# Kernel optimization log

Measured on AMD Instinct MI355X. Metric: run time of the kernel, lower is better.

## Reference

```python
import jax, jax.numpy as jnp
import numpy as np

PAD = 1  # symmetric spatial padding (pad_H == pad_W enforced by the module)


def setup_inputs() -> dict:
    key = jax.random.key(0)
    k1, k2, k3 = jax.random.split(key, 3)
    N, C, F, H, W, HH, WW = 32, 128, 128, 32, 32, 3, 3
    x = jax.random.normal(k1, (N, C, H, W), dtype=jnp.float32)
    weight = jax.random.normal(k2, (F, C, HH, WW), dtype=jnp.float32) * 0.05
    bias = jax.random.normal(k3, (F,), dtype=jnp.float32) * 0.05
    return {"x": x, "weight": weight, "bias": bias}


def reference(x, weight, bias):
    # Conv2dfft forward, no compression (compress_rate=0, preserve_energy=100,
    # next_power2=False, stride=1, real_fft path).
    N, C, H, W = x.shape
    F, _, HH, WW = weight.shape
    pad = PAD
    out_H = H - HH + 1 + 2 * pad
    out_W = W - WW + 1 + 2 * pad
    HHH = max(out_H, HH)
    WWW = max(out_W, WW)
    init_H = H + 2 * pad + HHH - 1  # full linear-conv FFT size
    init_W = W + 2 * pad + WWW - 1
    # torch_pad(input, (pad_W, pad_W + fft_pad_W, pad_H, pad_H + fft_pad_H))
    xp = jnp.pad(x, ((0, 0), (0, 0), (pad, init_H - pad - H), (pad, init_W - pad - W)))
    # torch_pad(filter, (0, fft_pad_W, 0, fft_pad_H))
    wp = jnp.pad(weight, ((0, 0), (0, 0), (0, init_H - HH), (0, init_W - WW)))
    xf = jnp.fft.rfft2(xp)          # [N, C, init_H, init_W//2+1] complex
    wf = jnp.fft.rfft2(wp)          # [F, C, init_H, init_W//2+1] complex
    # Cross-correlation in frequency domain: xfft * conj(yfft), contracted
    # over input channels C per frequency bin. This is exactly the math of the
    # module's fast_multiply (3-real-mult complex product via matmul) applied
    # to the conjugated filter spectrum.
    of = jnp.einsum('nchw,fchw->nfhw', xf, jnp.conj(wf))
    out = jnp.fft.irfft2(of, s=(init_H, init_W))[..., :out_H, :out_W]
    return out + bias[None, :, None, None]
```

## Files before the change

kernel.cpp:

```cpp
#include <hip/hip_runtime.h>


typedef short bf16x8 __attribute__((ext_vector_type(8)));
typedef short bf16x4 __attribute__((ext_vector_type(4)));
typedef float f32x4  __attribute__((ext_vector_type(4)));

__device__ __forceinline__ short f2bf(float f) {
  unsigned u = __builtin_bit_cast(unsigned, f);
  u = (u + 0x7fffu + ((u >> 16) & 1u)) >> 16;
  return (short)u;
}

__global__ __launch_bounds__(256) void conv_wprep(const float* __restrict__ w,
                                                  short* __restrict__ bc2) {
  int tid = blockIdx.x * 256 + threadIdx.x;
  float v = w[tid];
  int f   = tid / 1152;
  int rem = tid - f * 1152;
  int c   = rem / 9;
  int tap = rem - c * 9;
  int dst = ((((c >> 5) * 9 + tap) * 8 + (f >> 4)) * 512)
          + (((c >> 3) & 3) * 16 + (f & 15)) * 8
          + (c & 7);
  bc2[dst] = f2bf(v);
}

__device__ __forceinline__ void load_af(bf16x8* dst, const short* __restrict__ bc2,
                                        int chunk, int p, int fsel, int lane) {
  const short* base = bc2 + (((chunk * 9 + p * 3) * 8 + fsel * 4) * 512) + lane * 8;
#pragma unroll
  for (int q = 0; q < 3; ++q)
#pragma unroll
    for (int mt = 0; mt < 4; ++mt)
      dst[q * 4 + mt] = *(const bf16x8*)(base + (q * 8 + mt) * 512);
}

__global__ __launch_bounds__(256, 2) void conv_main(
    const float* __restrict__ x, const short* __restrict__ bc2,
    const float* __restrict__ bias, float* __restrict__ out) {
  __shared__ __align__(16) short xs[2][4 * 34 * 40];

  const int t    = threadIdx.x;
  const int lane = t & 63;
  const int wv   = t >> 6;
  const int n_img = blockIdx.x >> 4;
  const int h0    = (blockIdx.x & 15) << 1;

  const int l15  = lane & 15;
  const int quad = lane >> 4;
  const int fsel  = wv & 1;
  const int f_off = fsel * 64;
  const int s_row = wv >> 1;

  const int w_ = t & 31;
  const int g  = t >> 5;
  const float* xb = x + n_img * 128 * 1024;

  bf16x8 afA[12], afB[12];
  load_af(afA, bc2, 0, 0, fsel, lane);

  if (t < 128) {
    int buf = t >> 6, rem = t & 63;
    int r = rem >> 4, rem2 = rem & 15;
    int colsel = rem2 >> 3, q4 = rem2 & 7;
    *(int2*)&xs[buf][(r * 34 + colsel * 33) * 40 + q4 * 4] = make_int2(0, 0);
  }

  f32x4 acc[4][2] = {};
  float xv[16];

#pragma unroll
  for (int i = 0; i < 4; ++i) {
    int idx = i * 8 + g;
    int r = idx >> 3, cq = idx & 7;
    int hr = h0 - 1 + r;
    bool ok = (unsigned)hr < 32u;
#pragma unroll
    for (int cc = 0; cc < 4; ++cc)
      xv[i * 4 + cc] = ok ? xb[(cq * 4 + cc) * 1024 + hr * 32 + w_] : 0.f;
  }
#pragma unroll
  for (int i = 0; i < 4; ++i) {
    int idx = i * 8 + g;
    int r = idx >> 3, cq = idx & 7;
    bf16x4 v = { f2bf(xv[i*4+0]), f2bf(xv[i*4+1]), f2bf(xv[i*4+2]), f2bf(xv[i*4+3]) };
    *(bf16x4*)&xs[0][(r * 34 + w_ + 1) * 40 + cq * 4] = v;
  }
  __syncthreads();

#pragma unroll
  for (int chunk = 0; chunk < 4; ++chunk) {
    if (chunk < 3) {
#pragma unroll
      for (int i = 0; i < 4; ++i) {
        int idx = i * 8 + g;
        int r = idx >> 3, cq = idx & 7;
        int hr = h0 - 1 + r;
        bool ok = (unsigned)hr < 32u;
#pragma unroll
        for (int cc = 0; cc < 4; ++cc)
          xv[i * 4 + cc] =
              ok ? xb[((chunk + 1) * 32 + cq * 4 + cc) * 1024 + hr * 32 + w_] : 0.f;
      }
    }
    const short* xbuf = xs[chunk & 1];
#pragma unroll
    for (int p = 0; p < 3; ++p) {
      const int grp = chunk * 3 + p;
      const bf16x8* cur = (grp & 1) ? afB : afA;
      bf16x8*       nxt = (grp & 1) ? afA : afB;
      if (grp < 11)
        load_af(nxt, bc2, (grp + 1) / 3, (grp + 1) % 3, fsel, lane);
#pragma unroll
      for (int q = 0; q < 3; ++q) {
        bf16x8 bfr[2];
#pragma unroll
        for (int nt = 0; nt < 2; ++nt) {
          int r   = s_row + p;
          int col = nt * 16 + l15 + q;
          bfr[nt] = *(const bf16x8*)&xbuf[(r * 34 + col) * 40 + quad * 8];
        }
#pragma unroll
        for (int mt = 0; mt < 4; ++mt)
#pragma unroll
          for (int nt = 0; nt < 2; ++nt)
            acc[mt][nt] = __builtin_amdgcn_mfma_f32_16x16x32_bf16(
                cur[q * 4 + mt], bfr[nt], acc[mt][nt], 0, 0, 0);
      }
    }
    if (chunk < 3) {
#pragma unroll
      for (int i = 0; i < 4; ++i) {
        int idx = i * 8 + g;
        int r = idx >> 3, cq = idx & 7;
        bf16x4 v = { f2bf(xv[i*4+0]), f2bf(xv[i*4+1]), f2bf(xv[i*4+2]), f2bf(xv[i*4+3]) };
        *(bf16x4*)&xs[(chunk + 1) & 1][(r * 34 + w_ + 1) * 40 + cq * 4] = v;
      }
      __syncthreads();
    }
  }

  const int h = h0 + s_row;
#pragma unroll
  for (int nt = 0; nt < 2; ++nt) {
    int w_out = nt * 16 + l15;
#pragma unroll
    for (int mt = 0; mt < 4; ++mt) {
#pragma unroll
      for (int reg = 0; reg < 4; ++reg) {
        int f = f_off + mt * 16 + quad * 4 + reg;
        out[((n_img * 128 + f) * 32 + h) * 32 + w_out] = acc[mt][nt][reg] + bias[f];
      }
    }
  }
}

extern "C" void kernel_launch(void* const* d_in, const int* in_sizes, int n_in,
                              void* d_out, int out_size, void* d_ws, size_t ws_size,
                              hipStream_t stream) {
  const float* x    = (const float*)d_in[0];
  const float* w    = (const float*)d_in[1];
  const float* bias = (const float*)d_in[2];
  float* out = (float*)d_out;
  short* bc2 = (short*)d_ws;

  conv_wprep<<<576, 256, 0, stream>>>(w, bc2);
  conv_main<<<512, 256, 0, stream>>>(x, bc2, bias, out);
}
```

Baseline: 87.17 us.

## Pre-pad input to bf16 in a prep pass and stream tiles via global_load_lds

A merged prep kernel now converts weights and also writes a padded bf16 copy of the input laid out as per-row LDS images. The main conv kernel fills its double-buffered LDS tiles with direct global-to-LDS 16-byte loads, instead of loading fp32 into registers, converting and storing. This removes conversion work and register pressure from the main loop and merges the two prep launches into one. The cost is an extra write and read of the intermediate bf16 input through global memory.

```diff
diff --git a/kernel.cpp b/kernel.cpp
--- a/kernel.cpp
+++ b/kernel.cpp
@@ -11,18 +11,55 @@
   return (short)u;
 }
 
-__global__ __launch_bounds__(256) void conv_wprep(const float* __restrict__ w,
-                                                  short* __restrict__ bc2) {
-  int tid = blockIdx.x * 256 + threadIdx.x;
-  float v = w[tid];
-  int f   = tid / 1152;
-  int rem = tid - f * 1152;
-  int c   = rem / 9;
-  int tap = rem - c * 9;
-  int dst = ((((c >> 5) * 9 + tap) * 8 + (f >> 4)) * 512)
-          + (((c >> 3) & 3) * 16 + (f & 15)) * 8
-          + (c & 7);
-  bc2[dst] = f2bf(v);
+__device__ __forceinline__ void gload_lds16(const void* g, void* l) {
+  using gptr_t = const __attribute__((address_space(1))) unsigned int*;
+  using lptr_t = __attribute__((address_space(3))) unsigned int*;
+  __builtin_amdgcn_global_load_lds((gptr_t)(unsigned long long)g,
+                                   (lptr_t)(unsigned int)(unsigned long long)l,
+                                   16, 0, 0);
+}
+
+
+__global__ __launch_bounds__(256) void conv_prep(const float* __restrict__ x,
+                                                 const float* __restrict__ w,
+                                                 short* __restrict__ bc2,
+                                                 short* __restrict__ xp) {
+  const int b = blockIdx.x;
+  const int t = threadIdx.x;
+  if (b >= 4352) {
+    int tid = (b - 4352) * 256 + t;
+    float v = w[tid];
+    int f   = tid / 1152;
+    int rem = tid - f * 1152;
+    int c   = rem / 9;
+    int tap = rem - c * 9;
+    int dst = ((((c >> 5) * 9 + tap) * 8 + (f >> 4)) * 512)
+            + (((c >> 3) & 3) * 16 + (f & 15)) * 8
+            + (c & 7);
+    bc2[dst] = f2bf(v);
+    return;
+  }
+  const int xr = b % 34;
+  const int nc = b / 34;
+  const int n = nc >> 2, chunk = nc & 3;
+  short* row = xp + (size_t)b * 1536;
+  if (t < 16) {
+    bf16x4 z = {0, 0, 0, 0};
+    *(bf16x4*)&row[((t >> 3) ? 33 : 0) * 40 + (t & 7) * 4] = z;
+  }
+  const int h  = xr - 1;
+  const int w_ = t & 31;
+  const int g  = t >> 5;
+  bf16x4 v = {0, 0, 0, 0};
+  if ((unsigned)h < 32u) {
+    const float* src = x + (((size_t)(n * 128 + chunk * 32 + g * 4)) << 10)
+                         + h * 32 + w_;
+    v[0] = f2bf(src[0]);
+    v[1] = f2bf(src[1024]);
+    v[2] = f2bf(src[2048]);
+    v[3] = f2bf(src[3072]);
+  }
+  *(bf16x4*)&row[(w_ + 1) * 40 + g * 4] = v;
 }
 
 __device__ __forceinline__ void load_af(bf16x8* dst, const short* __restrict__ bc2,
@@ -36,9 +73,9 @@
 }
 
 __global__ __launch_bounds__(256, 2) void conv_main(
-    const float* __restrict__ x, const short* __restrict__ bc2,
+    const short* __restrict__ xp, const short* __restrict__ bc2,
     const float* __restrict__ bias, float* __restrict__ out) {
-  __shared__ __align__(16) short xs[2][4 * 34 * 40];
+  __shared__ __align__(16) short xs[2][6144];
 
   const int t    = threadIdx.x;
   const int lane = t & 63;
@@ -52,56 +89,32 @@
   const int f_off = fsel * 64;
   const int s_row = wv >> 1;
 
-  const int w_ = t & 31;
-  const int g  = t >> 5;
-  const float* xb = x + n_img * 128 * 1024;
+  const int go = wv * 1024 + lane * 16;
+  const int lo = wv * 1024;
 
   bf16x8 afA[12], afB[12];
   load_af(afA, bc2, 0, 0, fsel, lane);
 
-  if (t < 128) {
-    int buf = t >> 6, rem = t & 63;
-    int r = rem >> 4, rem2 = rem & 15;
-    int colsel = rem2 >> 3, q4 = rem2 & 7;
-    *(int2*)&xs[buf][(r * 34 + colsel * 33) * 40 + q4 * 4] = make_int2(0, 0);
+  {
+    const char* src = (const char*)(xp + ((size_t)(n_img * 4 + 0) * 34 + h0) * 1536);
+    char* dst = (char*)&xs[0][0];
+#pragma unroll
+    for (int rnd = 0; rnd < 3; ++rnd)
+      gload_lds16(src + rnd * 4096 + go, dst + rnd * 4096 + lo);
   }
 
   f32x4 acc[4][2] = {};
-  float xv[16];
-
-#pragma unroll
-  for (int i = 0; i < 4; ++i) {
-    int idx = i * 8 + g;
-    int r = idx >> 3, cq = idx & 7;
-    int hr = h0 - 1 + r;
-    bool ok = (unsigned)hr < 32u;
-#pragma unroll
-    for (int cc = 0; cc < 4; ++cc)
-      xv[i * 4 + cc] = ok ? xb[(cq * 4 + cc) * 1024 + hr * 32 + w_] : 0.f;
-  }
-#pragma unroll
-  for (int i = 0; i < 4; ++i) {
-    int idx = i * 8 + g;
-    int r = idx >> 3, cq = idx & 7;
-    bf16x4 v = { f2bf(xv[i*4+0]), f2bf(xv[i*4+1]), f2bf(xv[i*4+2]), f2bf(xv[i*4+3]) };
-    *(bf16x4*)&xs[0][(r * 34 + w_ + 1) * 40 + cq * 4] = v;
-  }
   __syncthreads();
 
 #pragma unroll
   for (int chunk = 0; chunk < 4; ++chunk) {
     if (chunk < 3) {
+      const char* src =
+          (const char*)(xp + ((size_t)(n_img * 4 + chunk + 1) * 34 + h0) * 1536);
+      char* dst = (char*)&xs[(chunk + 1) & 1][0];
 #pragma unroll
-      for (int i = 0; i < 4; ++i) {
-        int idx = i * 8 + g;
-        int r = idx >> 3, cq = idx & 7;
-        int hr = h0 - 1 + r;
-        bool ok = (unsigned)hr < 32u;
-#pragma unroll
-        for (int cc = 0; cc < 4; ++cc)
-          xv[i * 4 + cc] =
-              ok ? xb[((chunk + 1) * 32 + cq * 4 + cc) * 1024 + hr * 32 + w_] : 0.f;
-      }
+      for (int rnd = 0; rnd < 3; ++rnd)
+        gload_lds16(src + rnd * 4096 + go, dst + rnd * 4096 + lo);
     }
     const short* xbuf = xs[chunk & 1];
 #pragma unroll
@@ -118,7 +131,7 @@
         for (int nt = 0; nt < 2; ++nt) {
           int r   = s_row + p;
           int col = nt * 16 + l15 + q;
-          bfr[nt] = *(const bf16x8*)&xbuf[(r * 34 + col) * 40 + quad * 8];
+          bfr[nt] = *(const bf16x8*)&xbuf[r * 1536 + col * 40 + quad * 8];
         }
 #pragma unroll
         for (int mt = 0; mt < 4; ++mt)
@@ -128,16 +141,7 @@
                 cur[q * 4 + mt], bfr[nt], acc[mt][nt], 0, 0, 0);
       }
     }
-    if (chunk < 3) {
-#pragma unroll
-      for (int i = 0; i < 4; ++i) {
-        int idx = i * 8 + g;
-        int r = idx >> 3, cq = idx & 7;
-        bf16x4 v = { f2bf(xv[i*4+0]), f2bf(xv[i*4+1]), f2bf(xv[i*4+2]), f2bf(xv[i*4+3]) };
-        *(bf16x4*)&xs[(chunk + 1) & 1][(r * 34 + w_ + 1) * 40 + cq * 4] = v;
-      }
-      __syncthreads();
-    }
+    if (chunk < 3) __syncthreads();
   }
 
   const int h = h0 + s_row;
@@ -149,7 +153,8 @@
 #pragma unroll
       for (int reg = 0; reg < 4; ++reg) {
         int f = f_off + mt * 16 + quad * 4 + reg;
-        out[((n_img * 128 + f) * 32 + h) * 32 + w_out] = acc[mt][nt][reg] + bias[f];
+        out[(((size_t)n_img * 128 + f) * 32 + h) * 32 + w_out] =
+            acc[mt][nt][reg] + bias[f];
       }
     }
   }
@@ -163,7 +168,8 @@
   const float* bias = (const float*)d_in[2];
   float* out = (float*)d_out;
   short* bc2 = (short*)d_ws;
+  short* xp  = bc2 + 147456;
 
-  conv_wprep<<<576, 256, 0, stream>>>(w, bc2);
-  conv_main<<<512, 256, 0, stream>>>(x, bc2, bias, out);
+  conv_prep<<<4928, 256, 0, stream>>>(x, w, bc2, xp);
+  conv_main<<<512, 256, 0, stream>>>(xp, bc2, bias, out);
 }
```

Result: slower. 97.69 us (+12.1%).

## Shrink per-block tile to one output row and double the grid

Applied to the files above, without the earlier changes.

Each block now computes a single output row instead of two. The four waves split work as two filter halves by two column halves, rather than two filter halves by two rows. The grid doubles to 1024 blocks, LDS per block shrinks to 3 halo rows, accumulators per wave halve, and launch bounds raise the occupancy target to 3 blocks per CU. The aim is more parallelism and better latency hiding. In exchange, each block reloads the full weight fragments for half as much output, doubling weight traffic from L2, and the halo overhead per row grows (3 input rows per output row instead of 2).

```diff
diff --git a/kernel.cpp b/kernel.cpp
--- a/kernel.cpp
+++ b/kernel.cpp
@@ -35,22 +35,22 @@
       dst[q * 4 + mt] = *(const bf16x8*)(base + (q * 8 + mt) * 512);
 }
 
-__global__ __launch_bounds__(256, 2) void conv_main(
+__global__ __launch_bounds__(256, 3) void conv_main(
     const float* __restrict__ x, const short* __restrict__ bc2,
     const float* __restrict__ bias, float* __restrict__ out) {
-  __shared__ __align__(16) short xs[2][4 * 34 * 40];
+  __shared__ __align__(16) short xs[2][3 * 34 * 40];
 
   const int t    = threadIdx.x;
   const int lane = t & 63;
   const int wv   = t >> 6;
-  const int n_img = blockIdx.x >> 4;
-  const int h0    = (blockIdx.x & 15) << 1;
+  const int n_img = blockIdx.x >> 5;
+  const int h0    = blockIdx.x & 31;
 
   const int l15  = lane & 15;
   const int quad = lane >> 4;
   const int fsel  = wv & 1;
   const int f_off = fsel * 64;
-  const int s_row = wv >> 1;
+  const int chalf = wv >> 1;
 
   const int w_ = t & 31;
   const int g  = t >> 5;
@@ -59,18 +59,18 @@
   bf16x8 afA[12], afB[12];
   load_af(afA, bc2, 0, 0, fsel, lane);
 
-  if (t < 128) {
-    int buf = t >> 6, rem = t & 63;
+  if (t < 96) {
+    int buf = t / 48, rem = t % 48;
     int r = rem >> 4, rem2 = rem & 15;
     int colsel = rem2 >> 3, q4 = rem2 & 7;
     *(int2*)&xs[buf][(r * 34 + colsel * 33) * 40 + q4 * 4] = make_int2(0, 0);
   }
 
-  f32x4 acc[4][2] = {};
-  float xv[16];
+  f32x4 acc[4] = {};
+  float xv[12];
 
 #pragma unroll
-  for (int i = 0; i < 4; ++i) {
+  for (int i = 0; i < 3; ++i) {
     int idx = i * 8 + g;
     int r = idx >> 3, cq = idx & 7;
     int hr = h0 - 1 + r;
@@ -80,7 +80,7 @@
       xv[i * 4 + cc] = ok ? xb[(cq * 4 + cc) * 1024 + hr * 32 + w_] : 0.f;
   }
 #pragma unroll
-  for (int i = 0; i < 4; ++i) {
+  for (int i = 0; i < 3; ++i) {
     int idx = i * 8 + g;
     int r = idx >> 3, cq = idx & 7;
     bf16x4 v = { f2bf(xv[i*4+0]), f2bf(xv[i*4+1]), f2bf(xv[i*4+2]), f2bf(xv[i*4+3]) };
@@ -92,7 +92,7 @@
   for (int chunk = 0; chunk < 4; ++chunk) {
     if (chunk < 3) {
 #pragma unroll
-      for (int i = 0; i < 4; ++i) {
+      for (int i = 0; i < 3; ++i) {
         int idx = i * 8 + g;
         int r = idx >> 3, cq = idx & 7;
         int hr = h0 - 1 + r;
@@ -113,24 +113,17 @@
         load_af(nxt, bc2, (grp + 1) / 3, (grp + 1) % 3, fsel, lane);
 #pragma unroll
       for (int q = 0; q < 3; ++q) {
-        bf16x8 bfr[2];
-#pragma unroll
-        for (int nt = 0; nt < 2; ++nt) {
-          int r   = s_row + p;
-          int col = nt * 16 + l15 + q;
-          bfr[nt] = *(const bf16x8*)&xbuf[(r * 34 + col) * 40 + quad * 8];
-        }
+        int col = chalf * 16 + l15 + q;
+        bf16x8 bfr = *(const bf16x8*)&xbuf[(p * 34 + col) * 40 + quad * 8];
 #pragma unroll
         for (int mt = 0; mt < 4; ++mt)
-#pragma unroll
-          for (int nt = 0; nt < 2; ++nt)
-            acc[mt][nt] = __builtin_amdgcn_mfma_f32_16x16x32_bf16(
-                cur[q * 4 + mt], bfr[nt], acc[mt][nt], 0, 0, 0);
+          acc[mt] = __builtin_amdgcn_mfma_f32_16x16x32_bf16(
+              cur[q * 4 + mt], bfr, acc[mt], 0, 0, 0);
       }
     }
     if (chunk < 3) {
 #pragma unroll
-      for (int i = 0; i < 4; ++i) {
+      for (int i = 0; i < 3; ++i) {
         int idx = i * 8 + g;
         int r = idx >> 3, cq = idx & 7;
         bf16x4 v = { f2bf(xv[i*4+0]), f2bf(xv[i*4+1]), f2bf(xv[i*4+2]), f2bf(xv[i*4+3]) };
@@ -140,17 +133,14 @@
     }
   }
 
-  const int h = h0 + s_row;
+  const int w_out = chalf * 16 + l15;
 #pragma unroll
-  for (int nt = 0; nt < 2; ++nt) {
-    int w_out = nt * 16 + l15;
+  for (int mt = 0; mt < 4; ++mt) {
 #pragma unroll
-    for (int mt = 0; mt < 4; ++mt) {
-#pragma unroll
-      for (int reg = 0; reg < 4; ++reg) {
-        int f = f_off + mt * 16 + quad * 4 + reg;
-        out[((n_img * 128 + f) * 32 + h) * 32 + w_out] = acc[mt][nt][reg] + bias[f];
-      }
+    for (int reg = 0; reg < 4; ++reg) {
+      int f = f_off + mt * 16 + quad * 4 + reg;
+      out[(((size_t)n_img * 128 + f) * 32 + h0) * 32 + w_out] =
+          acc[mt][reg] + bias[f];
     }
   }
 }
@@ -165,5 +155,5 @@
   short* bc2 = (short*)d_ws;
 
   conv_wprep<<<576, 256, 0, stream>>>(w, bc2);
-  conv_main<<<512, 256, 0, stream>>>(x, bc2, bias, out);
+  conv_main<<<1024, 256, 0, stream>>>(x, bc2, bias, out);
 }
```

After: 92.44 us. 6.0% more time.

## Stage weight fragments in LDS via async global_load_lds double buffering

Applied to the files above, without the earlier changes.

Weight fragments were loaded by each wave straight into a register double buffer. They are now copied with asynchronous global-to-LDS DMA into a block-shared LDS double buffer, one group ahead, and each wave reads its fragments from LDS. The x-tile prefetch and store are reorganised so a barrier follows every tap group instead of every channel chunk. This removes duplicate weight loads across waves and frees registers. In exchange it uses much more LDS, adds more __syncthreads, and relies on correct waitcnt handling for the LDS DMA.

```diff
diff --git a/kernel.cpp b/kernel.cpp
--- a/kernel.cpp
+++ b/kernel.cpp
@@ -9,6 +9,14 @@
   unsigned u = __builtin_bit_cast(unsigned, f);
   u = (u + 0x7fffu + ((u >> 16) & 1u)) >> 16;
   return (short)u;
+}
+
+__device__ __forceinline__ void gload_lds16(const void* g, void* l) {
+  using gptr_t = const __attribute__((address_space(1))) unsigned int*;
+  using lptr_t = __attribute__((address_space(3))) unsigned int*;
+  __builtin_amdgcn_global_load_lds((gptr_t)(unsigned long long)g,
+                                   (lptr_t)(unsigned int)(unsigned long long)l,
+                                   16, 0, 0);
 }
 
 __global__ __launch_bounds__(256) void conv_wprep(const float* __restrict__ w,
@@ -25,20 +33,11 @@
   bc2[dst] = f2bf(v);
 }
 
-__device__ __forceinline__ void load_af(bf16x8* dst, const short* __restrict__ bc2,
-                                        int chunk, int p, int fsel, int lane) {
-  const short* base = bc2 + (((chunk * 9 + p * 3) * 8 + fsel * 4) * 512) + lane * 8;
-#pragma unroll
-  for (int q = 0; q < 3; ++q)
-#pragma unroll
-    for (int mt = 0; mt < 4; ++mt)
-      dst[q * 4 + mt] = *(const bf16x8*)(base + (q * 8 + mt) * 512);
-}
-
 __global__ __launch_bounds__(256, 2) void conv_main(
     const float* __restrict__ x, const short* __restrict__ bc2,
     const float* __restrict__ bias, float* __restrict__ out) {
   __shared__ __align__(16) short xs[2][4 * 34 * 40];
+  __shared__ __align__(16) short afl[2][12288];
 
   const int t    = threadIdx.x;
   const int lane = t & 63;
@@ -56,8 +55,14 @@
   const int g  = t >> 5;
   const float* xb = x + n_img * 128 * 1024;
 
-  bf16x8 afA[12], afB[12];
-  load_af(afA, bc2, 0, 0, fsel, lane);
+  const char* bc2b = (const char*)bc2 + t * 16;
+
+  {
+    char* dst = (char*)&afl[0][0] + wv * 1024;
+#pragma unroll
+    for (int r = 0; r < 6; ++r)
+      gload_lds16(bc2b + r * 4096, dst + r * 4096);
+  }
 
   if (t < 128) {
     int buf = t >> 6, rem = t & 63;
@@ -90,27 +95,38 @@
 
 #pragma unroll
   for (int chunk = 0; chunk < 4; ++chunk) {
-    if (chunk < 3) {
-#pragma unroll
-      for (int i = 0; i < 4; ++i) {
-        int idx = i * 8 + g;
-        int r = idx >> 3, cq = idx & 7;
-        int hr = h0 - 1 + r;
-        bool ok = (unsigned)hr < 32u;
-#pragma unroll
-        for (int cc = 0; cc < 4; ++cc)
-          xv[i * 4 + cc] =
-              ok ? xb[((chunk + 1) * 32 + cq * 4 + cc) * 1024 + hr * 32 + w_] : 0.f;
-      }
-    }
-    const short* xbuf = xs[chunk & 1];
 #pragma unroll
     for (int p = 0; p < 3; ++p) {
       const int grp = chunk * 3 + p;
-      const bf16x8* cur = (grp & 1) ? afB : afA;
-      bf16x8*       nxt = (grp & 1) ? afA : afB;
-      if (grp < 11)
-        load_af(nxt, bc2, (grp + 1) / 3, (grp + 1) % 3, fsel, lane);
+      if (grp < 11) {
+        const char* src = bc2b + (grp + 1) * 24576;
+        char* dst = (char*)&afl[(grp + 1) & 1][0] + wv * 1024;
+#pragma unroll
+        for (int r = 0; r < 6; ++r)
+          gload_lds16(src + r * 4096, dst + r * 4096);
+      }
+      if (p == 0 && chunk < 3) {
+#pragma unroll
+        for (int i = 0; i < 4; ++i) {
+          int idx = i * 8 + g;
+          int r = idx >> 3, cq = idx & 7;
+          int hr = h0 - 1 + r;
+          bool ok = (unsigned)hr < 32u;
+#pragma unroll
+          for (int cc = 0; cc < 4; ++cc)
+            xv[i * 4 + cc] =
+                ok ? xb[((chunk + 1) * 32 + cq * 4 + cc) * 1024 + hr * 32 + w_] : 0.f;
+        }
+      }
+      const short* xbuf = xs[chunk & 1];
+      const short* afb  = afl[grp & 1];
+      bf16x8 af[12];
+#pragma unroll
+      for (int q = 0; q < 3; ++q)
+#pragma unroll
+        for (int mt = 0; mt < 4; ++mt)
+          af[q * 4 + mt] =
+              *(const bf16x8*)&afb[(q * 8 + fsel * 4 + mt) * 512 + lane * 8];
 #pragma unroll
       for (int q = 0; q < 3; ++q) {
         bf16x8 bfr[2];
@@ -125,18 +141,18 @@
 #pragma unroll
           for (int nt = 0; nt < 2; ++nt)
             acc[mt][nt] = __builtin_amdgcn_mfma_f32_16x16x32_bf16(
-                cur[q * 4 + mt], bfr[nt], acc[mt][nt], 0, 0, 0);
+                af[q * 4 + mt], bfr[nt], acc[mt][nt], 0, 0, 0);
       }
-    }
-    if (chunk < 3) {
+      if (p == 2 && chunk < 3) {
 #pragma unroll
-      for (int i = 0; i < 4; ++i) {
-        int idx = i * 8 + g;
-        int r = idx >> 3, cq = idx & 7;
-        bf16x4 v = { f2bf(xv[i*4+0]), f2bf(xv[i*4+1]), f2bf(xv[i*4+2]), f2bf(xv[i*4+3]) };
-        *(bf16x4*)&xs[(chunk + 1) & 1][(r * 34 + w_ + 1) * 40 + cq * 4] = v;
+        for (int i = 0; i < 4; ++i) {
+          int idx = i * 8 + g;
+          int r = idx >> 3, cq = idx & 7;
+          bf16x4 v = { f2bf(xv[i*4+0]), f2bf(xv[i*4+1]), f2bf(xv[i*4+2]), f2bf(xv[i*4+3]) };
+          *(bf16x4*)&xs[(chunk + 1) & 1][(r * 34 + w_ + 1) * 40 + cq * 4] = v;
+        }
       }
-      __syncthreads();
+      if (grp < 11) __syncthreads();
     }
   }
 
@@ -149,7 +165,8 @@
 #pragma unroll
       for (int reg = 0; reg < 4; ++reg) {
         int f = f_off + mt * 16 + quad * 4 + reg;
-        out[((n_img * 128 + f) * 32 + h) * 32 + w_out] = acc[mt][nt][reg] + bias[f];
+        out[(((size_t)n_img * 128 + f) * 32 + h) * 32 + w_out] =
+            acc[mt][nt][reg] + bias[f];
       }
     }
   }
```

Result: faster. 84.02 us (-3.6%).
